# Performance work log

Hardware: AMD Instinct MI355X
Metric: run time of the kernel (lower is better)

The kernel has to match this reference:

```python
import jax, jax.numpy as jnp
import numpy as np

D_MODEL = 1024
N_HEADS = 16
D_K = D_MODEL // N_HEADS


def setup_inputs() -> dict:
    key = jax.random.key(0)
    ks = jax.random.split(key, 10)
    s = 1.0 / np.sqrt(D_MODEL)
    def lin(k):
        kw, kb = jax.random.split(k)
        W = jax.random.uniform(kw, (D_MODEL, D_MODEL), jnp.float32, -s, s)
        b = jax.random.uniform(kb, (D_MODEL,), jnp.float32, -s, s)
        return W, b
    Wq, bq = lin(ks[0])
    Wk, bk = lin(ks[1])
    Wv, bv = lin(ks[2])
    Wo, bo = lin(ks[3])
    x = jax.random.normal(ks[4], (2, 2048, D_MODEL), jnp.float32)
    gamma = jnp.ones((D_MODEL,), jnp.float32)
    beta = jnp.zeros((D_MODEL,), jnp.float32)
    return {"x": x, "Wq": Wq, "bq": bq, "Wk": Wk, "bk": bk,
            "Wv": Wv, "bv": bv, "Wo": Wo, "bo": bo,
            "gamma": gamma, "beta": beta}


def _mha(x, Wq, bq, Wk, bk, Wv, bv, Wo, bo, gamma, beta):
    B, S, _ = x.shape
    residual = x
    # Linear uses y = x @ W.T + b (torch nn.Linear convention)
    q = (x @ Wq.T + bq).reshape(B, S, N_HEADS, D_K).transpose(0, 2, 1, 3)
    k = (x @ Wk.T + bk).reshape(B, S, N_HEADS, D_K).transpose(0, 2, 1, 3)
    v = (x @ Wv.T + bv).reshape(B, S, N_HEADS, D_K).transpose(0, 2, 1, 3)
    scores = jnp.einsum("bhqd,bhkd->bhqk", q, k) / jnp.sqrt(jnp.float32(D_K))
    attn = jax.nn.softmax(scores, axis=-1)
    out = jnp.einsum("bhqk,bhkd->bhqd", attn, v)
    out = out.transpose(0, 2, 1, 3).reshape(B, S, D_MODEL)
    out = out @ Wo.T + bo
    h = out + residual
    mu = jnp.mean(h, axis=-1, keepdims=True)
    var = jnp.var(h, axis=-1, keepdims=True)
    h = (h - mu) / jnp.sqrt(var + 1e-5) * gamma + beta
    return jnp.where(h >= 0, h, 0.01 * h)


def reference(x, Wq, bq, Wk, bk, Wv, bv, Wo, bo, gamma, beta):
    return _mha(x, Wq, bq, Wk, bk, Wv, bv, Wo, bo, gamma, beta)
```

## Files before the change

kernel.cpp:

```cpp
#include <hip/hip_runtime.h>

#define DM   1024
#define NH   16
#define DK   64
#define SEQ  2048
#define BATCH 2

typedef __attribute__((ext_vector_type(8))) short bf16x8;
typedef __attribute__((ext_vector_type(4))) float f32x4;
typedef __attribute__((ext_vector_type(16))) float f32x16;

__device__ __forceinline__ unsigned short f2bf(float f) {
    unsigned int u = __builtin_bit_cast(unsigned int, f);
    u += 0x7FFFu + ((u >> 16) & 1u);
    return (unsigned short)(u >> 16);
}

__global__ __launch_bounds__(256)
void cvt_kernel(const float* __restrict__ x,
                const float* __restrict__ wq, const float* __restrict__ wk,
                const float* __restrict__ wv, const float* __restrict__ wo,
                unsigned short* __restrict__ xb,
                unsigned short* __restrict__ wqkvb,
                unsigned short* __restrict__ wob)
{
    const int seg = blockIdx.y;
    const float* src;
    unsigned short* dst;
    int n;
    if (seg == 0)      { src = x;  dst = xb;                  n = 4 << 20; }
    else if (seg == 1) { src = wq; dst = wqkvb;               n = 1 << 20; }
    else if (seg == 2) { src = wk; dst = wqkvb + (1 << 20);   n = 1 << 20; }
    else if (seg == 3) { src = wv; dst = wqkvb + (2 << 20);   n = 1 << 20; }
    else               { src = wo; dst = wob;                 n = 1 << 20; }
    for (int i = (blockIdx.x * 256 + threadIdx.x) * 4; i < n; i += 1024 * 256 * 4) {
        const float4 v = *reinterpret_cast<const float4*>(&src[i]);
        ushort4 o;
        o.x = f2bf(v.x); o.y = f2bf(v.y); o.z = f2bf(v.z); o.w = f2bf(v.w);
        *reinterpret_cast<ushort4*>(&dst[i]) = o;
    }
}

template <int MODE, int BN>
__global__ __launch_bounds__(256)
void gemm2_kernel(const unsigned short* __restrict__ Ab,
                  const unsigned short* __restrict__ Wall,
                  const float* __restrict__ B0, const float* __restrict__ B1,
                  const float* __restrict__ B2,
                  unsigned short* __restrict__ q_ws,
                  unsigned short* __restrict__ k_ws,
                  unsigned short* __restrict__ vt_ws,
                  const float* __restrict__ resid,
                  float* __restrict__ h_ws)
{
    __shared__ unsigned short sA[128 * 32];
    __shared__ unsigned short sB[BN * 32];

    const int tid = threadIdx.x, lane = tid & 63, wid = tid >> 6;
    const int n0 = blockIdx.x * BN, m0 = blockIdx.y * 128;
    const int z  = (MODE == 0) ? blockIdx.z : 0;
    const unsigned short* W = Wall + (size_t)z * (1 << 20);
    const float* bias = (MODE == 0) ? (z == 0 ? B0 : (z == 1 ? B1 : B2)) : B0;

    const int g = lane >> 4, lq = lane & 15;
    const int wr = wid >> 1, wc = wid & 1;
    const int rA = lane >> 2;
    const int csh = (lane & 3) * 8;

    f32x4 acc[4][BN / 32] = {};

    for (int k0 = 0; k0 < DM; k0 += 32) {
        #pragma unroll
        for (int i = 0; i < 2; ++i) {
            const int c = wid * 2 + i;
            __builtin_amdgcn_global_load_lds(
                (const __attribute__((address_space(1))) unsigned int*)
                    &Ab[(size_t)(m0 + c * 16 + rA) * DM + k0 + csh],
                (__attribute__((address_space(3))) unsigned int*)&sA[c * 512],
                16, 0, 0);
        }
        #pragma unroll
        for (int i = 0; i < BN / 64; ++i) {
            const int c = wid * (BN / 64) + i;
            __builtin_amdgcn_global_load_lds(
                (const __attribute__((address_space(1))) unsigned int*)
                    &W[(size_t)(n0 + c * 16 + rA) * DM + k0 + csh],
                (__attribute__((address_space(3))) unsigned int*)&sB[c * 512],
                16, 0, 0);
        }
        __syncthreads();

        bf16x8 a[4], b[BN / 32];
        #pragma unroll
        for (int m = 0; m < 4; ++m)
            a[m] = *reinterpret_cast<const bf16x8*>(&sA[(wr * 64 + m * 16 + lq) * 32 + 8 * g]);
        #pragma unroll
        for (int n = 0; n < BN / 32; ++n)
            b[n] = *reinterpret_cast<const bf16x8*>(&sB[(wc * (BN / 2) + n * 16 + lq) * 32 + 8 * g]);
        #pragma unroll
        for (int m = 0; m < 4; ++m)
            #pragma unroll
            for (int n = 0; n < BN / 32; ++n)
                acc[m][n] = __builtin_amdgcn_mfma_f32_16x16x32_bf16(
                    a[m], b[n], acc[m][n], 0, 0, 0);
        __syncthreads();
    }

    #pragma unroll
    for (int m = 0; m < 4; ++m) {
        #pragma unroll
        for (int n = 0; n < BN / 32; ++n) {
            #pragma unroll
            for (int j = 0; j < 4; ++j) {
                const int row = m0 + wr * 64 + m * 16 + 4 * g + j;
                const int col = n0 + wc * (BN / 2) + n * 16 + lq;
                float v = acc[m][n][j] + bias[col];
                if constexpr (MODE == 0) {
                    const int b_ = row >> 11, s = row & (SEQ - 1);
                    const int hh = col >> 6,  d = col & (DK - 1);
                    if (z == 0)
                        q_ws[(((size_t)(b_ * NH + hh) * SEQ + s) << 6) + d] = f2bf(v * 0.18033688f);
                    else if (z == 1)
                        k_ws[(((size_t)(b_ * NH + hh) * SEQ + s) << 6) + d] = f2bf(v);
                    else
                        vt_ws[((size_t)(b_ * NH + hh) * DK + d) * SEQ + s] = f2bf(v);
                } else {
                    const size_t idx = (size_t)row * DM + col;
                    h_ws[idx] = v + resid[idx];
                }
            }
        }
    }
}

__global__ __launch_bounds__(256)
void attn_kernel(const unsigned short* __restrict__ q_ws,
                 const unsigned short* __restrict__ k_ws,
                 const unsigned short* __restrict__ vt_ws,
                 unsigned short* __restrict__ ao_ws)
{
    __shared__ unsigned short lds4[8][4096];

    const int tid = threadIdx.x;
    const int lane = tid & 63, wid = tid >> 6;
    const int l31 = lane & 31, h = lane >> 5;
    const int bh = blockIdx.y;
    const int q0 = blockIdx.x * 128;
    const int q  = q0 + wid * 32 + l31;

    const size_t qbase = ((size_t)bh * SEQ + q) * DK;
    bf16x8 qf[4];
    #pragma unroll
    for (int j = 0; j < 4; ++j)
        qf[j] = *reinterpret_cast<const bf16x8*>(&q_ws[qbase + j * 16 + h * 8]);

    const short one_bf = (short)0x3F80;
    const bf16x8 onesf = {one_bf, one_bf, one_bf, one_bf, one_bf, one_bf, one_bf, one_bf};

    const int l8 = lane >> 3, l7 = lane & 7;
    const int scol = 8 * (l7 ^ l8);
    const unsigned short* kp0 = &k_ws [((size_t)bh * SEQ + wid * 16 + l8) * DK + scol];
    const unsigned short* kp1 = kp0 + 8 * DK;
    const unsigned short* vp0 = &vt_ws[((size_t)bh * DK  + wid * 16 + l8) * SEQ + scol];
    const unsigned short* vp1 = vp0 + 8 * SEQ;

    const int r7 = l31 & 7;
    const unsigned short* pK[4];
    const unsigned short* pV[4];
    #pragma unroll
    for (int j = 0; j < 4; ++j) {
        const int ck = 8 * (((j << 1) + h) ^ r7);
        pK[j] = &lds4[0][l31 * 64 + ck];
        pV[j] = &lds4[4][l31 * 64 + ck];
    }

    f32x16 oacc[2] = {};
    f32x16 lacc = {};

    const int dst0 = wid * 2 * 512, dst1 = (wid * 2 + 1) * 512;

    auto stage = [&](int kbuf) {
        __builtin_amdgcn_global_load_lds(
            (const __attribute__((address_space(1))) unsigned int*)kp0,
            (__attribute__((address_space(3))) unsigned int*)&lds4[kbuf][dst0], 16, 0, 0);
        __builtin_amdgcn_global_load_lds(
            (const __attribute__((address_space(1))) unsigned int*)kp1,
            (__attribute__((address_space(3))) unsigned int*)&lds4[kbuf][dst1], 16, 0, 0);
        __builtin_amdgcn_global_load_lds(
            (const __attribute__((address_space(1))) unsigned int*)vp0,
            (__attribute__((address_space(3))) unsigned int*)&lds4[4 + kbuf][dst0], 16, 0, 0);
        __builtin_amdgcn_global_load_lds(
            (const __attribute__((address_space(1))) unsigned int*)vp1,
            (__attribute__((address_space(3))) unsigned int*)&lds4[4 + kbuf][dst1], 16, 0, 0);
        kp0 += 64 * DK; kp1 += 64 * DK;
        vp0 += 64;      vp1 += 64;
    };

    auto compute = [&](int OFF) {
        f32x16 st0 = {}, st1 = {};
        __builtin_amdgcn_s_setprio(1);
        #pragma unroll
        for (int j = 0; j < 4; ++j) {
            const bf16x8 k0 = *reinterpret_cast<const bf16x8*>(pK[j] + OFF);
            const bf16x8 k1 = *reinterpret_cast<const bf16x8*>(pK[j] + OFF + 2048);
            st0 = __builtin_amdgcn_mfma_f32_32x32x16_bf16(k0, qf[j], st0, 0, 0, 0);
            st1 = __builtin_amdgcn_mfma_f32_32x32x16_bf16(k1, qf[j], st1, 0, 0, 0);
        }
        __builtin_amdgcn_s_setprio(0);

        bf16x8 pb[4];
        #pragma unroll
        for (int s = 0; s < 2; ++s) {
            #pragma unroll
            for (int jg = 0; jg < 2; ++jg) {
                const int rb = 8 * jg;
                float e0, e1, e2, e3, e4, e5, e6, e7;
                if (s == 0) {
                    e0 = exp2f(st0[rb + 0]); e1 = exp2f(st0[rb + 1]);
                    e2 = exp2f(st0[rb + 2]); e3 = exp2f(st0[rb + 3]);
                    e4 = exp2f(st0[rb + 4]); e5 = exp2f(st0[rb + 5]);
                    e6 = exp2f(st0[rb + 6]); e7 = exp2f(st0[rb + 7]);
                } else {
                    e0 = exp2f(st1[rb + 0]); e1 = exp2f(st1[rb + 1]);
                    e2 = exp2f(st1[rb + 2]); e3 = exp2f(st1[rb + 3]);
                    e4 = exp2f(st1[rb + 4]); e5 = exp2f(st1[rb + 5]);
                    e6 = exp2f(st1[rb + 6]); e7 = exp2f(st1[rb + 7]);
                }
                unsigned int wA, wB, wC, wD;
                asm("v_cvt_pk_bf16_f32 %0, %1, %2" : "=v"(wA) : "v"(e0), "v"(e1));
                asm("v_cvt_pk_bf16_f32 %0, %1, %2" : "=v"(wB) : "v"(e2), "v"(e3));
                asm("v_cvt_pk_bf16_f32 %0, %1, %2" : "=v"(wC) : "v"(e4), "v"(e5));
                asm("v_cvt_pk_bf16_f32 %0, %1, %2" : "=v"(wD) : "v"(e6), "v"(e7));
                asm("v_permlane32_swap_b32 %0, %1" : "+v"(wA), "+v"(wC));
                asm("v_permlane32_swap_b32 %0, %1" : "+v"(wB), "+v"(wD));
                uint4 ww;
                ww.x = wA; ww.y = wB; ww.z = wC; ww.w = wD;
                pb[2 * s + jg] = __builtin_bit_cast(bf16x8, ww);
            }
        }

        __builtin_amdgcn_s_setprio(1);
        #pragma unroll
        for (int jg = 0; jg < 4; ++jg)
            lacc = __builtin_amdgcn_mfma_f32_32x32x16_bf16(onesf, pb[jg], lacc, 0, 0, 0);
        #pragma unroll
        for (int dt = 0; dt < 2; ++dt)
            #pragma unroll
            for (int jg = 0; jg < 4; ++jg) {
                const bf16x8 vv = *reinterpret_cast<const bf16x8*>(pV[jg] + OFF + dt * 2048);
                oacc[dt] = __builtin_amdgcn_mfma_f32_32x32x16_bf16(vv, pb[jg], oacc[dt], 0, 0, 0);
            }
        __builtin_amdgcn_s_setprio(0);
    };

    stage(0);
    stage(1);
    __syncthreads();

    #pragma unroll 1
    for (int tt = 0; tt < 7; ++tt) {
        stage(2); stage(3);
        compute(0); compute(4096);
        __syncthreads();
        stage(0); stage(1);
        compute(8192); compute(12288);
        __syncthreads();
    }

    stage(2); stage(3);
    compute(0); compute(4096);
    __syncthreads();
    compute(8192); compute(12288);

    const int b_ = bh >> 4, hh = bh & 15;
    const float rl = 1.0f / lacc[0];
    unsigned short* aop = &ao_ws[(size_t)(b_ * SEQ + q) * DM + hh * 64];
    #pragma unroll
    for (int dt = 0; dt < 2; ++dt) {
        #pragma unroll
        for (int qd = 0; qd < 4; ++qd) {
            ushort4 o;
            o.x = f2bf(oacc[dt][4 * qd + 0] * rl);
            o.y = f2bf(oacc[dt][4 * qd + 1] * rl);
            o.z = f2bf(oacc[dt][4 * qd + 2] * rl);
            o.w = f2bf(oacc[dt][4 * qd + 3] * rl);
            *reinterpret_cast<ushort4*>(&aop[dt * 32 + 8 * qd + 4 * h]) = o;
        }
    }
}

__global__ __launch_bounds__(256)
void ln_kernel(const float* __restrict__ h, const float* __restrict__ gamma,
               const float* __restrict__ beta, float* __restrict__ out)
{
    __shared__ float s1[4], s2[4];
    const int row = blockIdx.x, tid = threadIdx.x;
    const float4 v = reinterpret_cast<const float4*>(h + (size_t)row * DM)[tid];
    float sum = v.x + v.y + v.z + v.w;
    float sq  = v.x * v.x + v.y * v.y + v.z * v.z + v.w * v.w;
    #pragma unroll
    for (int mk = 1; mk <= 32; mk <<= 1) {
        sum += __shfl_xor(sum, mk);
        sq  += __shfl_xor(sq, mk);
    }
    if ((tid & 63) == 0) { s1[tid >> 6] = sum; s2[tid >> 6] = sq; }
    __syncthreads();
    sum = s1[0] + s1[1] + s1[2] + s1[3];
    sq  = s2[0] + s2[1] + s2[2] + s2[3];
    const float mu = sum * (1.f / DM);
    const float var = sq * (1.f / DM) - mu * mu;
    const float rstd = rsqrtf(var + 1e-5f);
    const float4 gv = reinterpret_cast<const float4*>(gamma)[tid];
    const float4 bv = reinterpret_cast<const float4*>(beta)[tid];
    float4 o;
    o.x = (v.x - mu) * rstd * gv.x + bv.x;
    o.y = (v.y - mu) * rstd * gv.y + bv.y;
    o.z = (v.z - mu) * rstd * gv.z + bv.z;
    o.w = (v.w - mu) * rstd * gv.w + bv.w;
    o.x = o.x >= 0.f ? o.x : 0.01f * o.x;
    o.y = o.y >= 0.f ? o.y : 0.01f * o.y;
    o.z = o.z >= 0.f ? o.z : 0.01f * o.z;
    o.w = o.w >= 0.f ? o.w : 0.01f * o.w;
    reinterpret_cast<float4*>(out + (size_t)row * DM)[tid] = o;
}

extern "C" void kernel_launch(void* const* d_in, const int* in_sizes, int n_in,
                              void* d_out, int out_size, void* d_ws, size_t ws_size,
                              hipStream_t stream)
{
    const float* x     = (const float*)d_in[0];
    const float* Wq    = (const float*)d_in[1];
    const float* bq    = (const float*)d_in[2];
    const float* Wk    = (const float*)d_in[3];
    const float* bk    = (const float*)d_in[4];
    const float* Wv    = (const float*)d_in[5];
    const float* bv    = (const float*)d_in[6];
    const float* Wo    = (const float*)d_in[7];
    const float* bo    = (const float*)d_in[8];
    const float* gamma = (const float*)d_in[9];
    const float* beta  = (const float*)d_in[10];

    char* ws = (char*)d_ws;
    unsigned short* q_ws   = (unsigned short*)(ws);
    unsigned short* k_ws   = (unsigned short*)(ws + (8u << 20));
    unsigned short* vt_ws  = (unsigned short*)(ws + (16u << 20));
    unsigned short* ao_ws  = (unsigned short*)(ws + (24u << 20));
    unsigned short* xb_ws  = (unsigned short*)(ws + (32u << 20));
    unsigned short* wqkv_b = (unsigned short*)(ws + (40u << 20));
    unsigned short* wo_b   = (unsigned short*)(ws + (46u << 20));
    float* h_ws = (float*)ws;

    const dim3 blk(256);
    cvt_kernel<<<dim3(1024, 5), blk, 0, stream>>>(
        x, Wq, Wk, Wv, Wo, xb_ws, wqkv_b, wo_b);
    gemm2_kernel<0, 128><<<dim3(8, 32, 3), blk, 0, stream>>>(
        xb_ws, wqkv_b, bq, bk, bv, q_ws, k_ws, vt_ws, nullptr, nullptr);
    attn_kernel<<<dim3(16, 32), blk, 0, stream>>>(q_ws, k_ws, vt_ws, ao_ws);
    gemm2_kernel<1, 64><<<dim3(16, 32, 1), blk, 0, stream>>>(
        ao_ws, wo_b, bo, nullptr, nullptr, nullptr, nullptr, nullptr, x, h_ws);
    ln_kernel<<<dim3(4096), blk, 0, stream>>>(h_ws, gamma, beta, (float*)d_out);
}
```

Before: 137.5 us.

## Split attention key range across two wave groups and merge partial sums in LDS

The attention block grows from 256 to 512 threads. Two groups of four waves each process half of the key/value sequence for the same 128 queries, each using its own double-buffered LDS region. At the end the partial output and row-sum accumulators are combined through LDS before normalization and store. It also swaps exp2f for the raw v_exp_f32 instruction. The split doubles the waves available for latency hiding and halves each wave's serial loop, at the cost of a shallower prefetch pipeline, higher register pressure from the 512-thread launch bound, and an extra LDS reduction.

```diff
diff --git a/kernel.cpp b/kernel.cpp
--- a/kernel.cpp
+++ b/kernel.cpp
@@ -133,7 +133,7 @@
     }
 }
 
-__global__ __launch_bounds__(256)
+__global__ __launch_bounds__(512)
 void attn_kernel(const unsigned short* __restrict__ q_ws,
                  const unsigned short* __restrict__ k_ws,
                  const unsigned short* __restrict__ vt_ws,
@@ -143,10 +143,11 @@
 
     const int tid = threadIdx.x;
     const int lane = tid & 63, wid = tid >> 6;
+    const int s = wid >> 2, w4 = wid & 3;
     const int l31 = lane & 31, h = lane >> 5;
     const int bh = blockIdx.y;
     const int q0 = blockIdx.x * 128;
-    const int q  = q0 + wid * 32 + l31;
+    const int q  = q0 + w4 * 32 + l31;
 
     const size_t qbase = ((size_t)bh * SEQ + q) * DK;
     bf16x8 qf[4];
@@ -159,9 +160,9 @@
 
     const int l8 = lane >> 3, l7 = lane & 7;
     const int scol = 8 * (l7 ^ l8);
-    const unsigned short* kp0 = &k_ws [((size_t)bh * SEQ + wid * 16 + l8) * DK + scol];
+    const unsigned short* kp0 = &k_ws [((size_t)bh * SEQ + s * 1024 + w4 * 16 + l8) * DK + scol];
     const unsigned short* kp1 = kp0 + 8 * DK;
-    const unsigned short* vp0 = &vt_ws[((size_t)bh * DK  + wid * 16 + l8) * SEQ + scol];
+    const unsigned short* vp0 = &vt_ws[((size_t)bh * DK + w4 * 16 + l8) * SEQ + s * 1024 + scol];
     const unsigned short* vp1 = vp0 + 8 * SEQ;
 
     const int r7 = l31 & 7;
@@ -170,28 +171,28 @@
     #pragma unroll
     for (int j = 0; j < 4; ++j) {
         const int ck = 8 * (((j << 1) + h) ^ r7);
-        pK[j] = &lds4[0][l31 * 64 + ck];
-        pV[j] = &lds4[4][l31 * 64 + ck];
+        pK[j] = &lds4[2 * s][l31 * 64 + ck];
+        pV[j] = &lds4[4 + 2 * s][l31 * 64 + ck];
     }
 
     f32x16 oacc[2] = {};
     f32x16 lacc = {};
 
-    const int dst0 = wid * 2 * 512, dst1 = (wid * 2 + 1) * 512;
-
-    auto stage = [&](int kbuf) {
+    const int dst0 = w4 * 2 * 512, dst1 = (w4 * 2 + 1) * 512;
+
+    auto stage = [&](int b) {
         __builtin_amdgcn_global_load_lds(
             (const __attribute__((address_space(1))) unsigned int*)kp0,
-            (__attribute__((address_space(3))) unsigned int*)&lds4[kbuf][dst0], 16, 0, 0);
+            (__attribute__((address_space(3))) unsigned int*)&lds4[2 * s + b][dst0], 16, 0, 0);
         __builtin_amdgcn_global_load_lds(
             (const __attribute__((address_space(1))) unsigned int*)kp1,
-            (__attribute__((address_space(3))) unsigned int*)&lds4[kbuf][dst1], 16, 0, 0);
+            (__attribute__((address_space(3))) unsigned int*)&lds4[2 * s + b][dst1], 16, 0, 0);
         __builtin_amdgcn_global_load_lds(
             (const __attribute__((address_space(1))) unsigned int*)vp0,
-            (__attribute__((address_space(3))) unsigned int*)&lds4[4 + kbuf][dst0], 16, 0, 0);
+            (__attribute__((address_space(3))) unsigned int*)&lds4[4 + 2 * s + b][dst0], 16, 0, 0);
         __builtin_amdgcn_global_load_lds(
             (const __attribute__((address_space(1))) unsigned int*)vp1,
-            (__attribute__((address_space(3))) unsigned int*)&lds4[4 + kbuf][dst1], 16, 0, 0);
+            (__attribute__((address_space(3))) unsigned int*)&lds4[4 + 2 * s + b][dst1], 16, 0, 0);
         kp0 += 64 * DK; kp1 += 64 * DK;
         vp0 += 64;      vp1 += 64;
     };
@@ -210,22 +211,24 @@
 
         bf16x8 pb[4];
         #pragma unroll
-        for (int s = 0; s < 2; ++s) {
+        for (int ss = 0; ss < 2; ++ss) {
             #pragma unroll
             for (int jg = 0; jg < 2; ++jg) {
                 const int rb = 8 * jg;
                 float e0, e1, e2, e3, e4, e5, e6, e7;
-                if (s == 0) {
-                    e0 = exp2f(st0[rb + 0]); e1 = exp2f(st0[rb + 1]);
-                    e2 = exp2f(st0[rb + 2]); e3 = exp2f(st0[rb + 3]);
-                    e4 = exp2f(st0[rb + 4]); e5 = exp2f(st0[rb + 5]);
-                    e6 = exp2f(st0[rb + 6]); e7 = exp2f(st0[rb + 7]);
+                #define EXP2(dst, src) asm("v_exp_f32 %0, %1" : "=v"(dst) : "v"(src))
+                if (ss == 0) {
+                    EXP2(e0, st0[rb + 0]); EXP2(e1, st0[rb + 1]);
+                    EXP2(e2, st0[rb + 2]); EXP2(e3, st0[rb + 3]);
+                    EXP2(e4, st0[rb + 4]); EXP2(e5, st0[rb + 5]);
+                    EXP2(e6, st0[rb + 6]); EXP2(e7, st0[rb + 7]);
                 } else {
-                    e0 = exp2f(st1[rb + 0]); e1 = exp2f(st1[rb + 1]);
-                    e2 = exp2f(st1[rb + 2]); e3 = exp2f(st1[rb + 3]);
-                    e4 = exp2f(st1[rb + 4]); e5 = exp2f(st1[rb + 5]);
-                    e6 = exp2f(st1[rb + 6]); e7 = exp2f(st1[rb + 7]);
+                    EXP2(e0, st1[rb + 0]); EXP2(e1, st1[rb + 1]);
+                    EXP2(e2, st1[rb + 2]); EXP2(e3, st1[rb + 3]);
+                    EXP2(e4, st1[rb + 4]); EXP2(e5, st1[rb + 5]);
+                    EXP2(e6, st1[rb + 6]); EXP2(e7, st1[rb + 7]);
                 }
+                #undef EXP2
                 unsigned int wA, wB, wC, wD;
                 asm("v_cvt_pk_bf16_f32 %0, %1, %2" : "=v"(wA) : "v"(e0), "v"(e1));
                 asm("v_cvt_pk_bf16_f32 %0, %1, %2" : "=v"(wB) : "v"(e2), "v"(e3));
@@ -235,7 +238,7 @@
                 asm("v_permlane32_swap_b32 %0, %1" : "+v"(wB), "+v"(wD));
                 uint4 ww;
                 ww.x = wA; ww.y = wB; ww.z = wC; ww.w = wD;
-                pb[2 * s + jg] = __builtin_bit_cast(bf16x8, ww);
+                pb[2 * ss + jg] = __builtin_bit_cast(bf16x8, ww);
             }
         }
 
@@ -254,37 +257,48 @@
     };
 
     stage(0);
-    stage(1);
     __syncthreads();
-
     #pragma unroll 1
-    for (int tt = 0; tt < 7; ++tt) {
-        stage(2); stage(3);
-        compute(0); compute(4096);
+    for (int tt = 0; tt < 8; ++tt) {
+        stage(1);
+        compute(0);
         __syncthreads();
-        stage(0); stage(1);
-        compute(8192); compute(12288);
+        if (tt < 7) stage(0);
+        compute(4096);
         __syncthreads();
     }
 
-    stage(2); stage(3);
-    compute(0); compute(4096);
+    float* fl = (float*)&lds4[0][0];
+    if (s == 1) {
+        float* p = fl + (size_t)(w4 * 64 + lane) * 33;
+        #pragma unroll
+        for (int dt = 0; dt < 2; ++dt)
+            #pragma unroll
+            for (int r = 0; r < 16; ++r) p[dt * 16 + r] = oacc[dt][r];
+        p[32] = lacc[0];
+    }
     __syncthreads();
-    compute(8192); compute(12288);
-
-    const int b_ = bh >> 4, hh = bh & 15;
-    const float rl = 1.0f / lacc[0];
-    unsigned short* aop = &ao_ws[(size_t)(b_ * SEQ + q) * DM + hh * 64];
-    #pragma unroll
-    for (int dt = 0; dt < 2; ++dt) {
-        #pragma unroll
-        for (int qd = 0; qd < 4; ++qd) {
-            ushort4 o;
-            o.x = f2bf(oacc[dt][4 * qd + 0] * rl);
-            o.y = f2bf(oacc[dt][4 * qd + 1] * rl);
-            o.z = f2bf(oacc[dt][4 * qd + 2] * rl);
-            o.w = f2bf(oacc[dt][4 * qd + 3] * rl);
-            *reinterpret_cast<ushort4*>(&aop[dt * 32 + 8 * qd + 4 * h]) = o;
+    if (s == 0) {
+        const float* p = fl + (size_t)(w4 * 64 + lane) * 33;
+        #pragma unroll
+        for (int dt = 0; dt < 2; ++dt)
+            #pragma unroll
+            for (int r = 0; r < 16; ++r) oacc[dt][r] += p[dt * 16 + r];
+        const float rl = 1.0f / (lacc[0] + p[32]);
+
+        const int b_ = bh >> 4, hh = bh & 15;
+        unsigned short* aop = &ao_ws[(size_t)(b_ * SEQ + q) * DM + hh * 64];
+        #pragma unroll
+        for (int dt = 0; dt < 2; ++dt) {
+            #pragma unroll
+            for (int qd = 0; qd < 4; ++qd) {
+                ushort4 o;
+                o.x = f2bf(oacc[dt][4 * qd + 0] * rl);
+                o.y = f2bf(oacc[dt][4 * qd + 1] * rl);
+                o.z = f2bf(oacc[dt][4 * qd + 2] * rl);
+                o.w = f2bf(oacc[dt][4 * qd + 3] * rl);
+                *reinterpret_cast<ushort4*>(&aop[dt * 32 + 8 * qd + 4 * h]) = o;
+            }
         }
     }
 }
@@ -355,7 +369,7 @@
         x, Wq, Wk, Wv, Wo, xb_ws, wqkv_b, wo_b);
     gemm2_kernel<0, 128><<<dim3(8, 32, 3), blk, 0, stream>>>(
         xb_ws, wqkv_b, bq, bk, bv, q_ws, k_ws, vt_ws, nullptr, nullptr);
-    attn_kernel<<<dim3(16, 32), blk, 0, stream>>>(q_ws, k_ws, vt_ws, ao_ws);
+    attn_kernel<<<dim3(16, 32), dim3(512), 0, stream>>>(q_ws, k_ws, vt_ws, ao_ws);
     gemm2_kernel<1, 64><<<dim3(16, 32, 1), blk, 0, stream>>>(
         ao_ws, wo_b, bo, nullptr, nullptr, nullptr, nullptr, nullptr, x, h_ws);
     ln_kernel<<<dim3(4096), blk, 0, stream>>>(h_ws, gamma, beta, (float*)d_out);
```

Result: faster. 129.8 us (-5.6%).
